# Kernel optimization log

Hardware: AMD Instinct MI355X
Metric: run time of the kernel (lower is better)

Reference implementation:

```python
import jax, jax.numpy as jnp
import numpy as np


def _sobel_kernels():
    # Stack the four fixed 3x3 operators into one [4,1,3,3] OIHW kernel so
    # the four single-channel convs become a single 4-output-channel conv.
    f_x = [[-1, -2, -1], [0, 0, 0], [1, 2, 1]]
    f_y = [[-1, 0, 1], [-2, 0, 2], [-1, 0, 1]]
    f_tl_br = [[-2, -1, 0], [-1, 0, 1], [0, 1, 2]]
    f_tr_bl = [[0, -1, -2], [1, 0, -1], [2, 1, 0]]
    k = np.stack([f_x, f_y, f_tl_br, f_tr_bl]).astype(np.float32)  # [4,3,3]
    return jnp.asarray(k[:, None, :, :])  # [4,1,3,3]


def setup_inputs() -> dict:
    key = jax.random.key(0)
    lab = jax.random.normal(key, (64, 1, 512, 512), dtype=jnp.float32)
    return {"lab": lab, "kernels": _sobel_kernels()}


def reference(lab, kernels):
    # lab: [B,1,H,W]; kernels: [4,1,3,3]
    lab_l = lab.astype(jnp.float32)
    taps = jax.lax.conv_general_dilated(
        lab_l, kernels,
        window_strides=(1, 1), padding=((1, 1), (1, 1)),
        dimension_numbers=("NCHW", "OIHW", "NCHW"))  # [B,4,H,W]
    edge = jnp.sum(jnp.abs(taps), axis=1)  # [B,H,W]
    # edge[edge > 0] = 1 then .long(); abs-sum is >= 0 so this is a 0/1 map
    edge = jnp.where(edge > 0, 1, 0).astype(jnp.int32)
    return edge  # squeezed: channel dim already reduced
```

## Files before the change

kernel.cpp:

```cpp
#include <hip/hip_runtime.h>


#define IMG_W 512
#define IMG_H 512
#define R_ROWS 8
#define WSLOTS 6

struct Row {
  float4 lo, hi;
  float lft, rgt;
};

__device__ __forceinline__ float rget(const Row& r, int k) {
  switch (k) {
    case 0: return r.lft;
    case 1: return r.lo.x; case 2: return r.lo.y;
    case 3: return r.lo.z; case 4: return r.lo.w;
    case 5: return r.hi.x; case 6: return r.hi.y;
    case 7: return r.hi.z; case 8: return r.hi.w;
    default: return r.rgt;
  }
}

__device__ __forceinline__ void loadrow(Row& r, const float* img, int yy, int px) {
  int yc = min(max(yy, 0), IMG_H - 1);
  const float* p = img + yc * IMG_W + px;
  r.lo = *reinterpret_cast<const float4*>(p);
  r.hi = *reinterpret_cast<const float4*>(p + 4);
}

__device__ __forceinline__ void finishrow(Row& r, int yy, int lane) {
  float mask = ((unsigned)yy < (unsigned)IMG_H) ? 1.f : 0.f;
  r.lo.x *= mask; r.lo.y *= mask; r.lo.z *= mask; r.lo.w *= mask;
  r.hi.x *= mask; r.hi.y *= mask; r.hi.z *= mask; r.hi.w *= mask;
  float lf = __shfl_up(r.hi.w, 1);
  float rt = __shfl_down(r.lo.x, 1);
  r.lft = (lane == 0)  ? 0.f : lf;
  r.rgt = (lane == 63) ? 0.f : rt;
}

__device__ __forceinline__ void compute_store(const Row& T, const Row& M,
                                              const Row& B, int* orow) {
  int res[8];
#pragma unroll
  for (int j = 0; j < 8; ++j) {
    float t0 = rget(T, j), t1 = rget(T, j + 1), t2 = rget(T, j + 2);
    float m0 = rget(M, j),                      m2 = rget(M, j + 2);
    float b0 = rget(B, j), b1 = rget(B, j + 1), b2 = rget(B, j + 2);
    float tx = (b0 - t0) + 2.f * (b1 - t1) + (b2 - t2);
    float ty = (t2 - t0) + 2.f * (m2 - m0) + (b2 - b0);
    float d1 = -2.f * t0 - t1 - m0 + m2 + b1 + 2.f * b2;
    float d2 = -t1 - 2.f * t2 + m0 - m2 + 2.f * b0 + b1;
    float e = fabsf(tx) + fabsf(ty) + fabsf(d1) + fabsf(d2);
    res[j] = (e > 0.f) ? 1 : 0;
  }
  *reinterpret_cast<int4*>(orow)     = make_int4(res[0], res[1], res[2], res[3]);
  *reinterpret_cast<int4*>(orow + 4) = make_int4(res[4], res[5], res[6], res[7]);
}

__global__ __launch_bounds__(256, 4) void edgenet_kernel(
    const float* __restrict__ in, int* __restrict__ out) {
  const int lane = threadIdx.x & 63;
  const int wid  = threadIdx.x >> 6;
  const int b    = blockIdx.x >> 4;
  const int y0   = ((blockIdx.x & 15) << 5) + (wid << 3);
  const int px   = lane << 3;

  const float* img = in + (size_t)b * (IMG_H * IMG_W);
  int* orow = out + ((size_t)b * IMG_H + y0) * IMG_W + px;

  Row s[WSLOTS];
#pragma unroll
  for (int k = 0; k < WSLOTS; ++k) loadrow(s[k], img, y0 - 1 + k, px);
  finishrow(s[0], y0 - 1, lane);
  finishrow(s[1], y0,     lane);

#pragma unroll
  for (int i = 0; i < R_ROWS; ++i) {
    finishrow(s[(i + 2) % WSLOTS], y0 + i + 1, lane);
    compute_store(s[i % WSLOTS], s[(i + 1) % WSLOTS], s[(i + 2) % WSLOTS],
                  orow + i * IMG_W);
    if (i + 5 <= R_ROWS)
      loadrow(s[i % WSLOTS], img, y0 + i + 5, px);
  }
}

extern "C" void kernel_launch(void* const* d_in, const int* in_sizes, int n_in,
                              void* d_out, int out_size, void* d_ws, size_t ws_size,
                              hipStream_t stream) {
  const float* lab = (const float*)d_in[0];
  int* out = (int*)d_out;
  int blocks = 64 * (IMG_H / (4 * R_ROWS));
  edgenet_kernel<<<blocks, 256, 0, stream>>>(lab, out);
}
```

Before: 30.61 us.

## Stage 18-row image tiles in LDS and compute 16 output rows per block

Each block now cooperatively loads a 16-row tile plus halo rows into shared memory with coalesced float4 loads. Each wave then builds its rows from LDS and computes 4 output rows. This lowers redundant halo re-reads from global memory. In exchange it adds a block barrier, 36KB of LDS per block that limits occupancy, and drops the previous register-level software pipelining of loads.

Measured after the change: 28.50 us. -6.9%, faster.

```diff
diff --git a/kernel.cpp b/kernel.cpp
--- a/kernel.cpp
+++ b/kernel.cpp
@@ -3,8 +3,8 @@
 
 #define IMG_W 512
 #define IMG_H 512
-#define R_ROWS 8
-#define WSLOTS 6
+#define TROWS 16
+#define SROWS (TROWS + 2)
 
 struct Row {
   float4 lo, hi;
@@ -20,23 +20,6 @@
     case 7: return r.hi.z; case 8: return r.hi.w;
     default: return r.rgt;
   }
-}
-
-__device__ __forceinline__ void loadrow(Row& r, const float* img, int yy, int px) {
-  int yc = min(max(yy, 0), IMG_H - 1);
-  const float* p = img + yc * IMG_W + px;
-  r.lo = *reinterpret_cast<const float4*>(p);
-  r.hi = *reinterpret_cast<const float4*>(p + 4);
-}
-
-__device__ __forceinline__ void finishrow(Row& r, int yy, int lane) {
-  float mask = ((unsigned)yy < (unsigned)IMG_H) ? 1.f : 0.f;
-  r.lo.x *= mask; r.lo.y *= mask; r.lo.z *= mask; r.lo.w *= mask;
-  r.hi.x *= mask; r.hi.y *= mask; r.hi.z *= mask; r.hi.w *= mask;
-  float lf = __shfl_up(r.hi.w, 1);
-  float rt = __shfl_down(r.lo.x, 1);
-  r.lft = (lane == 0)  ? 0.f : lf;
-  r.rgt = (lane == 63) ? 0.f : rt;
 }
 
 __device__ __forceinline__ void compute_store(const Row& T, const Row& M,
@@ -58,30 +41,53 @@
   *reinterpret_cast<int4*>(orow + 4) = make_int4(res[4], res[5], res[6], res[7]);
 }
 
-__global__ __launch_bounds__(256, 4) void edgenet_kernel(
+__global__ __launch_bounds__(256) void edgenet_kernel(
     const float* __restrict__ in, int* __restrict__ out) {
-  const int lane = threadIdx.x & 63;
-  const int wid  = threadIdx.x >> 6;
-  const int b    = blockIdx.x >> 4;
-  const int y0   = ((blockIdx.x & 15) << 5) + (wid << 3);
-  const int px   = lane << 3;
-
+  __shared__ float lds[SROWS * IMG_W];
+  const int tid  = threadIdx.x;
+  const int lane = tid & 63;
+  const int wid  = tid >> 6;
+  const int b    = blockIdx.x >> 5;
+  const int t    = blockIdx.x & 31;
+  const int y0   = t << 4;
   const float* img = in + (size_t)b * (IMG_H * IMG_W);
-  int* orow = out + ((size_t)b * IMG_H + y0) * IMG_W + px;
-
-  Row s[WSLOTS];
-#pragma unroll
-  for (int k = 0; k < WSLOTS; ++k) loadrow(s[k], img, y0 - 1 + k, px);
-  finishrow(s[0], y0 - 1, lane);
-  finishrow(s[1], y0,     lane);
 
 #pragma unroll
-  for (int i = 0; i < R_ROWS; ++i) {
-    finishrow(s[(i + 2) % WSLOTS], y0 + i + 1, lane);
-    compute_store(s[i % WSLOTS], s[(i + 1) % WSLOTS], s[(i + 2) % WSLOTS],
-                  orow + i * IMG_W);
-    if (i + 5 <= R_ROWS)
-      loadrow(s[i % WSLOTS], img, y0 + i + 5, px);
+  for (int k = 0; k < 9; ++k) {
+    int idx = tid + (k << 8);
+    int lr  = idx >> 7;
+    int c   = (idx & 127) << 2;
+    int gy  = min(max(y0 + lr - 1, 0), IMG_H - 1);
+    float4 v = *reinterpret_cast<const float4*>(img + gy * IMG_W + c);
+    *reinterpret_cast<float4*>(&lds[lr * IMG_W + c]) = v;
+  }
+  __syncthreads();
+
+  const int r0 = wid << 2;
+
+  auto ldrow = [&](int lr, Row& r) {
+    const float* p = &lds[lr * IMG_W + (lane << 3)];
+    float4 lo = *reinterpret_cast<const float4*>(p);
+    float4 hi = *reinterpret_cast<const float4*>(p + 4);
+    float mk = ((unsigned)(y0 + lr - 1) < (unsigned)IMG_H) ? 1.f : 0.f;
+    lo.x *= mk; lo.y *= mk; lo.z *= mk; lo.w *= mk;
+    hi.x *= mk; hi.y *= mk; hi.z *= mk; hi.w *= mk;
+    r.lo = lo; r.hi = hi;
+    float lf = __shfl_up(hi.w, 1);
+    float rt = __shfl_down(lo.x, 1);
+    r.lft = (lane == 0)  ? 0.f : lf;
+    r.rgt = (lane == 63) ? 0.f : rt;
+  };
+
+  Row s[3];
+  ldrow(r0,     s[0]);
+  ldrow(r0 + 1, s[1]);
+  ldrow(r0 + 2, s[2]);
+  int* orow = out + ((size_t)b * IMG_H + y0 + r0) * IMG_W + (lane << 3);
+#pragma unroll
+  for (int i = 0; i < 4; ++i) {
+    compute_store(s[i % 3], s[(i + 1) % 3], s[(i + 2) % 3], orow + i * IMG_W);
+    if (i < 3) ldrow(r0 + i + 3, s[i % 3]);
   }
 }
 
@@ -90,6 +96,6 @@
                               hipStream_t stream) {
   const float* lab = (const float*)d_in[0];
   int* out = (int*)d_out;
-  int blocks = 64 * (IMG_H / (4 * R_ROWS));
+  int blocks = 64 * (IMG_H / TROWS);
   edgenet_kernel<<<blocks, 256, 0, stream>>>(lab, out);
 }
```
